# Kernel tuning notes

Measured on AMD Instinct MI355X. Metric: run time of the kernel, lower is better.

Reference implementation:

```python
import jax, jax.numpy as jnp
import numpy as np

E = 23   # unique experts
K = 3    # active experts per token

def setup_inputs() -> dict:
    key = jax.random.key(0)
    ks = jax.random.split(key, 11)
    d, h, B, N = 1024, 768, 16, 196
    s = 0.02  # init scale so sigmoid gate is non-saturated
    return {
        "x":      jax.random.normal(ks[0], (B, N, d), jnp.float32),
        "gate_w": jax.random.normal(ks[1], (d, E), jnp.float32) * s,
        "gate_b": jnp.zeros((E,), jnp.float32),
        "w1":     jax.random.normal(ks[2], (E, d, h), jnp.float32) * s,
        "b1":     jnp.zeros((E, h), jnp.float32),
        "w2":     jax.random.normal(ks[3], (E, h, d), jnp.float32) * s,
        "b2":     jnp.zeros((E, d), jnp.float32),
        "ws1":    jax.random.normal(ks[4], (d, h), jnp.float32) * s,
        "bs1":    jnp.zeros((h,), jnp.float32),
        "ws2":    jax.random.normal(ks[5], (h, d), jnp.float32) * s,
        "bs2":    jnp.zeros((d,), jnp.float32),
    }

def reference(x, gate_w, gate_b, w1, b1, w2, b2, ws1, bs1, ws2, bs2):
    o_shape = x.shape
    xt = x.reshape(-1, o_shape[-1])            # [T, d]
    T = xt.shape[0]

    # gating: sigmoid gate, top-3 (the 'bias' buffer in the source is zeros)
    gw = jax.nn.sigmoid(xt @ gate_w + gate_b)  # [T, E]
    top_vals, top_idx = jax.lax.top_k(gw, K)   # [T, K]
    tw = top_vals / top_vals.sum(-1, keepdims=True)

    # dense combine weights: tw scattered to [T, E] (0 for unselected experts)
    w_dense = jnp.zeros_like(gw).at[jnp.arange(T)[:, None], top_idx].add(tw)

    # expert MLPs (dense-masked equivalent of the grouped dispatch)
    hh = jax.nn.gelu(jnp.einsum('td,edh->teh', xt, w1) + b1, approximate=False)
    eo = jnp.einsum('teh,ehd->ted', hh, w2) + b2          # [T, E, d]

    # shared expert
    shared = jax.nn.gelu(xt @ ws1 + bs1, approximate=False) @ ws2 + bs2

    out = shared + jnp.einsum('ted,te->td', eo, w_dense)  # [T, d]

    # aux load-balancing loss
    gwn = gw / gw.sum(-1, keepdims=True)
    P = gwn.mean(0)                                       # [E]
    counts = jnp.zeros((E,), gw.dtype).at[top_idx.reshape(-1)].add(1.0)
    Fv = E * counts / (K * T)
    aux = (P * Fv).sum()

    return out.reshape(o_shape), aux
```

## Files before the change

### kernel.cpp

```cpp
#include <hip/hip_runtime.h>
#include <hip/hip_bf16.h>

#define T_TOK 3136
#define DDIM  1024
#define HDIM  768
#define NEXP  23
#define TOPK  3
#define MTILE 128
#define NTILE 128
#define KTILE 32
#define LDSB  40
#define MAXTILES 128
#define MAX_SLOTS 16384
#define GATE_BLOCKS 1568

typedef __attribute__((ext_vector_type(8))) short  short8;
typedef __attribute__((ext_vector_type(4))) short  short4v;
typedef __attribute__((ext_vector_type(4))) float  floatx4;

__device__ __forceinline__ short f2b(float f) {
    union { float f; unsigned u; } v; v.f = f;
    unsigned r = v.u + 0x7FFFu + ((v.u >> 16) & 1u);
    return (short)(r >> 16);
}
__device__ __forceinline__ float b2f(short s) {
    union { unsigned u; float f; } v; v.u = ((unsigned)(unsigned short)s) << 16; return v.f;
}
__device__ __forceinline__ float gelu_exact(float v) {
    return 0.5f * v * (1.0f + erff(v * 0.70710678118654752f));
}
__device__ __forceinline__ void gld16(const short* g, short* l) {
    __builtin_amdgcn_global_load_lds(
        (const __attribute__((address_space(1))) void*)g,
        (__attribute__((address_space(3))) void*)l, 16, 0, 0);
}

__global__ __launch_bounds__(256) void gwt_kernel(const float* __restrict__ gw, float* __restrict__ gwT) {
    __shared__ float tile[32][33];
    const int kt = blockIdx.x;
    const int tx = threadIdx.x & 31, ty = threadIdx.x >> 5;
    #pragma unroll
    for (int i = 0; i < 4; i++) {
        int k = ty + i * 8;
        tile[k][tx] = (tx < NEXP) ? gw[(size_t)(kt * 32 + k) * NEXP + tx] : 0.f;
    }
    __syncthreads();
    #pragma unroll
    for (int i = 0; i < 4; i++) {
        int e = ty + i * 8;
        if (e < 24) gwT[(size_t)e * DDIM + kt * 32 + tx] = tile[tx][e];
    }
}

__global__ __launch_bounds__(256) void xcvt_kernel(const float* __restrict__ x, short* __restrict__ xb) {
    int i = blockIdx.x * 256 + threadIdx.x;
    float4 v = ((const float4*)x)[i];
    short4v s = { f2b(v.x), f2b(v.y), f2b(v.z), f2b(v.w) };
    ((short4v*)xb)[i] = s;
}

__global__ __launch_bounds__(256) void gate_kernel(
    const float* __restrict__ x, const float* __restrict__ gwT, const float* __restrict__ gb,
    float* __restrict__ Pf, int* __restrict__ top_idx, float* __restrict__ top_w)
{
    const int tid = threadIdx.x;
    const int lane = tid & 63, wave = tid >> 6;
    const int ebase = wave * 6;
    __shared__ float sg[24];
    __shared__ float accP[NEXP];
    if (tid < NEXP) accP[tid] = 0.f;

    for (int t = blockIdx.x; t < T_TOK; t += GATE_BLOCKS) {
        const float4* xr4 = (const float4*)(x + (size_t)t * DDIM);
        float4 xv[4];
        #pragma unroll
        for (int j = 0; j < 4; j++) xv[j] = xr4[j * 64 + lane];

        double a0 = 0, a1 = 0, a2 = 0, a3 = 0, a4 = 0, a5 = 0;
        #pragma unroll
        for (int j = 0; j < 4; j++) {
            const float4* gp = (const float4*)gwT + (size_t)ebase * 256 + j * 64 + lane;
            float4 g0 = gp[0 * 256], g1 = gp[1 * 256], g2 = gp[2 * 256];
            float4 g3 = gp[3 * 256], g4 = gp[4 * 256], g5 = gp[5 * 256];
            float4 xj = xv[j];
            a0 += (double)xj.x * g0.x + (double)xj.y * g0.y + (double)xj.z * g0.z + (double)xj.w * g0.w;
            a1 += (double)xj.x * g1.x + (double)xj.y * g1.y + (double)xj.z * g1.z + (double)xj.w * g1.w;
            a2 += (double)xj.x * g2.x + (double)xj.y * g2.y + (double)xj.z * g2.z + (double)xj.w * g2.w;
            a3 += (double)xj.x * g3.x + (double)xj.y * g3.y + (double)xj.z * g3.z + (double)xj.w * g3.w;
            a4 += (double)xj.x * g4.x + (double)xj.y * g4.y + (double)xj.z * g4.z + (double)xj.w * g4.w;
            a5 += (double)xj.x * g5.x + (double)xj.y * g5.y + (double)xj.z * g5.z + (double)xj.w * g5.w;
        }
        #pragma unroll
        for (int off = 32; off > 0; off >>= 1) {
            a0 += __shfl_xor(a0, off);
            a1 += __shfl_xor(a1, off);
            a2 += __shfl_xor(a2, off);
            a3 += __shfl_xor(a3, off);
            a4 += __shfl_xor(a4, off);
            a5 += __shfl_xor(a5, off);
        }

        if (lane == 0) {
            double av[6] = { a0, a1, a2, a3, a4, a5 };
            #pragma unroll
            for (int i = 0; i < 6; i++) {
                int e = ebase + i;
                if (e < NEXP) {
                    float z = (float)av[i] + gb[e];
                    sg[e] = 1.0f / (1.0f + expf(-z));
                }
            }
        }
        __syncthreads();

        if (tid < NEXP) {
            float s = 0.f;
            #pragma unroll
            for (int e = 0; e < NEXP; e++) s += sg[e];
            accP[tid] += sg[tid] / s;
        }
        if (tid == 0) {
            float v0 = -1.f, v1 = -1.f, v2 = -1.f; int i0 = 0, i1 = 0, i2 = 0;
            for (int e = 0; e < NEXP; e++) {
                float v = sg[e];
                if (v > v0)      { v2 = v1; i2 = i1; v1 = v0; i1 = i0; v0 = v; i0 = e; }
                else if (v > v1) { v2 = v1; i2 = i1; v1 = v; i1 = e; }
                else if (v > v2) { v2 = v; i2 = e; }
            }
            float ts = v0 + v1 + v2;
            top_idx[t * 3 + 0] = i0; top_w[t * 3 + 0] = v0 / ts;
            top_idx[t * 3 + 1] = i1; top_w[t * 3 + 1] = v1 / ts;
            top_idx[t * 3 + 2] = i2; top_w[t * 3 + 2] = v2 / ts;
        }
        __syncthreads();
    }
    if (tid < NEXP) atomicAdd(&Pf[tid], accP[tid]);
}

__global__ __launch_bounds__(1024) void route_kernel(
    const int* __restrict__ top_idx, const float* __restrict__ Pf,
    int* __restrict__ ntl,
    int* __restrict__ slot_t, int* __restrict__ slot_of,
    int* __restrict__ tmap_e, int* __restrict__ tmap_b,
    float* __restrict__ out_aux)
{
    __shared__ int h[NEXP];
    __shared__ int lfill[NEXP];
    __shared__ int soffs[NEXP + 1];
    __shared__ int sntl[NEXP + 1];
    const int tid = threadIdx.x;
    if (tid < NEXP) { h[tid] = 0; lfill[tid] = 0; }
    __syncthreads();
    for (int i = tid; i < T_TOK * 3; i += 1024) atomicAdd(&h[top_idx[i]], 1);
    __syncthreads();
    if (tid == 0) {
        int o = 0, ti = 0;
        for (int e = 0; e < NEXP; e++) {
            int c = h[e];
            int nt = (c + MTILE - 1) / MTILE;
            soffs[e] = o; sntl[e] = nt; ntl[e] = nt;
            for (int j = 0; j < nt; j++) { tmap_e[ti] = e; tmap_b[ti] = o + j * MTILE; ti++; }
            o += nt * MTILE;
        }
        int nts = (T_TOK + MTILE - 1) / MTILE;
        soffs[NEXP] = o; sntl[NEXP] = nts; ntl[NEXP] = nts;
        for (int j = 0; j < nts; j++) { tmap_e[ti] = NEXP; tmap_b[ti] = o + j * MTILE; ti++; }
        ntl[NEXP + 1] = ti;
        float aux = 0.f;
        for (int e = 0; e < NEXP; e++) {
            float P = Pf[e] / (float)T_TOK;
            float F = (float)NEXP * (float)h[e] / (float)(TOPK * T_TOK);
            aux += P * F;
        }
        out_aux[0] = aux;
    }
    __syncthreads();
    for (int e = 0; e <= NEXP; e++) {
        int cnt = (e < NEXP) ? h[e] : T_TOK;
        int s0 = soffs[e] + cnt, s1 = soffs[e] + sntl[e] * MTILE;
        for (int s = s0 + tid; s < s1; s += 1024) slot_t[s] = 0;
    }
    for (int t = tid; t < T_TOK; t += 1024) {
        #pragma unroll
        for (int k = 0; k < TOPK; k++) {
            int e = top_idx[t * 3 + k];
            int pos = atomicAdd(&lfill[e], 1);
            int s = soffs[e] + pos;
            slot_t[s] = t;
            slot_of[t * 4 + k] = s;
        }
        int s = soffs[NEXP] + t;
        slot_t[s] = t;
        slot_of[t * 4 + 3] = s;
    }
}

__global__ __launch_bounds__(256) void gemm1_kernel(
    const short* __restrict__ xb,
    const float* __restrict__ w1, const float* __restrict__ b1,
    const float* __restrict__ ws1, const float* __restrict__ bs1,
    const int* __restrict__ tmap_e, const int* __restrict__ tmap_b,
    const int* __restrict__ ntl,
    const int* __restrict__ slot_t, short* __restrict__ hh)
{
    if ((int)blockIdx.y >= ntl[NEXP + 1]) return;
    const int e = tmap_e[blockIdx.y];
    const int slot_base = tmap_b[blockIdx.y];
    const int n0 = blockIdx.x * NTILE;
    const float* __restrict__ Wf = (e < NEXP) ? (w1 + (size_t)e * DDIM * HDIM) : ws1;
    const float* __restrict__ Bv = (e < NEXP) ? (b1 + (size_t)e * HDIM) : bs1;

    __shared__ __align__(16) short As[2][MTILE * KTILE];
    __shared__ __align__(16) short Bs[2][NTILE * LDSB];
    __shared__ int toks[MTILE];

    const int tid = threadIdx.x;
    for (int i = tid; i < MTILE; i += 256) toks[i] = slot_t[slot_base + i];

    const int lane = tid & 63, wave = tid >> 6;
    const int mbase = (wave & 1) * 64, nbase = (wave >> 1) * 64;
    const int lc = lane & 15, q = lane >> 4;
    const int xq8 = (q ^ ((lc >> 1) & 3)) << 3;

    const int srow = wave * 16 + (lane >> 2);
    const int c8   = (lane & 3) * 8;

    __syncthreads();
    const short* gA0 = xb + (size_t)toks[srow]      * DDIM + c8;
    const short* gA1 = xb + (size_t)toks[64 + srow] * DDIM + c8;
    const int lofs0 = wave * 512, lofs1 = 2048 + wave * 512;

    const int g = wave, cn = lane;
    const float* gW = Wf + (size_t)(8 * g) * HDIM + n0 + 2 * cn;
    const int bws = (g ^ (cn & 3)) << 3;
    const int bofs0 = (2 * cn) * LDSB + bws, bofs1 = (2 * cn + 1) * LDSB + bws;

    floatx4 acc[4][4];
    #pragma unroll
    for (int m = 0; m < 4; m++)
        #pragma unroll
        for (int n = 0; n < 4; n++) acc[m][n] = (floatx4)0.f;

    const int NT = DDIM / KTILE;
    float2 f[8];
    #pragma unroll
    for (int j = 0; j < 8; j++) f[j] = *(const float2*)(gW + (size_t)j * HDIM);
    gld16(gA0, &As[0][lofs0]);
    gld16(gA1, &As[0][lofs1]);
    {
        short8 s0, s1;
        #pragma unroll
        for (int j = 0; j < 8; j++) { s0[j] = f2b(f[j].x); s1[j] = f2b(f[j].y); }
        *(short8*)&Bs[0][bofs0] = s0;
        *(short8*)&Bs[0][bofs1] = s1;
    }
    #pragma unroll
    for (int j = 0; j < 8; j++) f[j] = *(const float2*)(gW + (size_t)(KTILE + j) * HDIM);
    __syncthreads();

    for (int t = 0; t < NT; t++) {
        const int cur = t & 1;
        if (t + 1 < NT) {
            gld16(gA0 + (t + 1) * KTILE, &As[cur ^ 1][lofs0]);
            gld16(gA1 + (t + 1) * KTILE, &As[cur ^ 1][lofs1]);
            short8 s0, s1;
            #pragma unroll
            for (int j = 0; j < 8; j++) { s0[j] = f2b(f[j].x); s1[j] = f2b(f[j].y); }
            *(short8*)&Bs[cur ^ 1][bofs0] = s0;
            *(short8*)&Bs[cur ^ 1][bofs1] = s1;
        }
        if (t + 2 < NT) {
            #pragma unroll
            for (int j = 0; j < 8; j++)
                f[j] = *(const float2*)(gW + (size_t)((t + 2) * KTILE + j) * HDIM);
        }
        short8 af[4], bf[4];
        #pragma unroll
        for (int m = 0; m < 4; m++) af[m] = *(const short8*)&As[cur][(mbase + m * 16 + lc) * KTILE + q * 8];
        #pragma unroll
        for (int n = 0; n < 4; n++) bf[n] = *(const short8*)&Bs[cur][(nbase + n * 16 + lc) * LDSB + xq8];
        #pragma unroll
        for (int m = 0; m < 4; m++)
            #pragma unroll
            for (int n = 0; n < 4; n++)
                acc[m][n] = __builtin_amdgcn_mfma_f32_16x16x32_bf16(af[m], bf[n], acc[m][n], 0, 0, 0);
        __syncthreads();
    }

    #pragma unroll
    for (int n = 0; n < 4; n++) {
        const int col = n0 + nbase + n * 16 + lc;
        const float bb = Bv[col];
        #pragma unroll
        for (int m = 0; m < 4; m++) {
            const int rbase = slot_base + mbase + m * 16 + q * 4;
            #pragma unroll
            for (int r = 0; r < 4; r++) {
                float v = acc[m][n][r] + bb;
                hh[(size_t)(rbase + r) * HDIM + col] = f2b(gelu_exact(v));
            }
        }
    }
}

__global__ __launch_bounds__(256) void gemm2_kernel(
    const short* __restrict__ hh,
    const float* __restrict__ w2, const float* __restrict__ b2,
    const float* __restrict__ ws2, const float* __restrict__ bs2,
    const int* __restrict__ tmap_e, const int* __restrict__ tmap_b,
    const int* __restrict__ ntl,
    short* __restrict__ eo)
{
    if ((int)blockIdx.y >= ntl[NEXP + 1]) return;
    const int e = tmap_e[blockIdx.y];
    const int slot_base = tmap_b[blockIdx.y];
    const int n0 = blockIdx.x * NTILE;
    const float* __restrict__ Wf = (e < NEXP) ? (w2 + (size_t)e * HDIM * DDIM) : ws2;
    const float* __restrict__ Bv = (e < NEXP) ? (b2 + (size_t)e * DDIM) : bs2;

    __shared__ __align__(16) short As[2][MTILE * KTILE];
    __shared__ __align__(16) short Bs[2][NTILE * LDSB];

    const int tid = threadIdx.x;
    const int lane = tid & 63, wave = tid >> 6;
    const int mbase = (wave & 1) * 64, nbase = (wave >> 1) * 64;
    const int lc = lane & 15, q = lane >> 4;
    const int xq8 = (q ^ ((lc >> 1) & 3)) << 3;

    const int srow = wave * 16 + (lane >> 2);
    const int c8   = (lane & 3) * 8;

    const short* gA0 = hh + (size_t)(slot_base + srow)      * HDIM + c8;
    const short* gA1 = hh + (size_t)(slot_base + 64 + srow) * HDIM + c8;
    const int lofs0 = wave * 512, lofs1 = 2048 + wave * 512;

    const int g = wave, cn = lane;
    const float* gW = Wf + (size_t)(8 * g) * DDIM + n0 + 2 * cn;
    const int bws = (g ^ (cn & 3)) << 3;
    const int bofs0 = (2 * cn) * LDSB + bws, bofs1 = (2 * cn + 1) * LDSB + bws;

    floatx4 acc[4][4];
    #pragma unroll
    for (int m = 0; m < 4; m++)
        #pragma unroll
        for (int n = 0; n < 4; n++) acc[m][n] = (floatx4)0.f;

    const int NT = HDIM / KTILE;
    float2 f[8];
    #pragma unroll
    for (int j = 0; j < 8; j++) f[j] = *(const float2*)(gW + (size_t)j * DDIM);
    gld16(gA0, &As[0][lofs0]);
    gld16(gA1, &As[0][lofs1]);
    {
        short8 s0, s1;
        #pragma unroll
        for (int j = 0; j < 8; j++) { s0[j] = f2b(f[j].x); s1[j] = f2b(f[j].y); }
        *(short8*)&Bs[0][bofs0] = s0;
        *(short8*)&Bs[0][bofs1] = s1;
    }
    #pragma unroll
    for (int j = 0; j < 8; j++) f[j] = *(const float2*)(gW + (size_t)(KTILE + j) * DDIM);
    __syncthreads();

    for (int t = 0; t < NT; t++) {
        const int cur = t & 1;
        if (t + 1 < NT) {
            gld16(gA0 + (t + 1) * KTILE, &As[cur ^ 1][lofs0]);
            gld16(gA1 + (t + 1) * KTILE, &As[cur ^ 1][lofs1]);
            short8 s0, s1;
            #pragma unroll
            for (int j = 0; j < 8; j++) { s0[j] = f2b(f[j].x); s1[j] = f2b(f[j].y); }
            *(short8*)&Bs[cur ^ 1][bofs0] = s0;
            *(short8*)&Bs[cur ^ 1][bofs1] = s1;
        }
        if (t + 2 < NT) {
            #pragma unroll
            for (int j = 0; j < 8; j++)
                f[j] = *(const float2*)(gW + (size_t)((t + 2) * KTILE + j) * DDIM);
        }
        short8 af[4], bf[4];
        #pragma unroll
        for (int m = 0; m < 4; m++) af[m] = *(const short8*)&As[cur][(mbase + m * 16 + lc) * KTILE + q * 8];
        #pragma unroll
        for (int n = 0; n < 4; n++) bf[n] = *(const short8*)&Bs[cur][(nbase + n * 16 + lc) * LDSB + xq8];
        #pragma unroll
        for (int m = 0; m < 4; m++)
            #pragma unroll
            for (int n = 0; n < 4; n++)
                acc[m][n] = __builtin_amdgcn_mfma_f32_16x16x32_bf16(af[m], bf[n], acc[m][n], 0, 0, 0);
        __syncthreads();
    }

    #pragma unroll
    for (int n = 0; n < 4; n++) {
        const int col = n0 + nbase + n * 16 + lc;
        const float bb = Bv[col];
        #pragma unroll
        for (int m = 0; m < 4; m++) {
            const int rbase = slot_base + mbase + m * 16 + q * 4;
            #pragma unroll
            for (int r = 0; r < 4; r++)
                eo[(size_t)(rbase + r) * DDIM + col] = f2b(acc[m][n][r] + bb);
        }
    }
}

__global__ __launch_bounds__(256) void combine_kernel(
    const short* __restrict__ eo, const float* __restrict__ top_w,
    const int* __restrict__ slot_of, float* __restrict__ out)
{
    const int t = blockIdx.x;
    const int c = threadIdx.x * 4;
    const int s0 = slot_of[t * 4 + 0], s1 = slot_of[t * 4 + 1];
    const int s2 = slot_of[t * 4 + 2], s3 = slot_of[t * 4 + 3];
    const float w0 = top_w[t * 3 + 0], w1 = top_w[t * 3 + 1], w2 = top_w[t * 3 + 2];
    short4v a = *(const short4v*)(eo + (size_t)s0 * DDIM + c);
    short4v b = *(const short4v*)(eo + (size_t)s1 * DDIM + c);
    short4v d = *(const short4v*)(eo + (size_t)s2 * DDIM + c);
    short4v s = *(const short4v*)(eo + (size_t)s3 * DDIM + c);
    float4 o;
    o.x = b2f(s.x) + w0 * b2f(a.x) + w1 * b2f(b.x) + w2 * b2f(d.x);
    o.y = b2f(s.y) + w0 * b2f(a.y) + w1 * b2f(b.y) + w2 * b2f(d.y);
    o.z = b2f(s.z) + w0 * b2f(a.z) + w1 * b2f(b.z) + w2 * b2f(d.z);
    o.w = b2f(s.w) + w0 * b2f(a.w) + w1 * b2f(b.w) + w2 * b2f(d.w);
    *(float4*)(out + (size_t)t * DDIM + c) = o;
}

extern "C" void kernel_launch(void* const* d_in, const int* in_sizes, int n_in,
                              void* d_out, int out_size, void* d_ws, size_t ws_size,
                              hipStream_t stream)
{
    const float* x   = (const float*)d_in[0];
    const float* gw  = (const float*)d_in[1];
    const float* gb  = (const float*)d_in[2];
    const float* w1  = (const float*)d_in[3];
    const float* b1  = (const float*)d_in[4];
    const float* w2  = (const float*)d_in[5];
    const float* b2  = (const float*)d_in[6];
    const float* ws1 = (const float*)d_in[7];
    const float* bs1 = (const float*)d_in[8];
    const float* ws2 = (const float*)d_in[9];
    const float* bs2 = (const float*)d_in[10];
    float* out = (float*)d_out;

    char* p = (char*)d_ws;
    auto alloc = [&](size_t bytes) -> char* {
        char* r = p; p += (bytes + 255) & ~(size_t)255; return r;
    };
    int*   top_idx  = (int*)  alloc((size_t)T_TOK * 3 * 4);
    float* top_w    = (float*)alloc((size_t)T_TOK * 3 * 4);
    float* Pf       = (float*)alloc(NEXP * 4);
    int*   ntl      = (int*)  alloc((NEXP + 2) * 4);
    int*   slot_t   = (int*)  alloc((size_t)MAX_SLOTS * 4);
    int*   slot_of  = (int*)  alloc((size_t)T_TOK * 4 * 4);
    int*   tmap_e   = (int*)  alloc((size_t)MAXTILES * 4);
    int*   tmap_b   = (int*)  alloc((size_t)MAXTILES * 4);
    float* gwT      = (float*)alloc((size_t)24 * DDIM * 4);
    short* xb       = (short*)alloc((size_t)T_TOK * DDIM * 2);
    short* hh       = (short*)alloc((size_t)MAX_SLOTS * HDIM * 2);
    short* eo       = (short*)alloc((size_t)MAX_SLOTS * DDIM * 2);

    hipMemsetAsync(Pf, 0, NEXP * 4, stream);

    gwt_kernel<<<DDIM / 32, 256, 0, stream>>>(gw, gwT);
    xcvt_kernel<<<(T_TOK * DDIM / 4) / 256, 256, 0, stream>>>(x, xb);
    gate_kernel<<<GATE_BLOCKS, 256, 0, stream>>>(x, gwT, gb, Pf, top_idx, top_w);
    route_kernel<<<1, 1024, 0, stream>>>(top_idx, Pf, ntl, slot_t, slot_of,
                                         tmap_e, tmap_b, out + (size_t)T_TOK * DDIM);
    gemm1_kernel<<<dim3(HDIM / NTILE, MAXTILES), 256, 0, stream>>>(
        xb, w1, b1, ws1, bs1, tmap_e, tmap_b, ntl, slot_t, hh);
    gemm2_kernel<<<dim3(DDIM / NTILE, MAXTILES), 256, 0, stream>>>(
        hh, w2, b2, ws2, bs2, tmap_e, tmap_b, ntl, eo);
    combine_kernel<<<T_TOK, 256, 0, stream>>>(eo, top_w, slot_of, out);
}
```

Measured before the change: 383.3 us.

## Double K-step per GEMM iteration and fuse prep kernels into one launch

Both expert GEMM kernels now process 64 K-elements per main-loop iteration as two 32-wide sub-tiles, halving the number of barriers and loop iterations and deepening the register prefetch of fp32 weights. The x-to-bf16 conversion and gate-weight transpose kernels are merged into a single launch to save one kernel launch. The change doubles LDS use per block and register pressure from the larger prefetch buffer, which may reduce occupancy.

```diff
diff --git a/kernel.cpp b/kernel.cpp
--- a/kernel.cpp
+++ b/kernel.cpp
@@ -9,10 +9,14 @@
 #define MTILE 128
 #define NTILE 128
 #define KTILE 32
+#define KSTEP 64
 #define LDSB  40
+#define ASUB  4096
+#define BSUB  5120
 #define MAXTILES 128
 #define MAX_SLOTS 16384
 #define GATE_BLOCKS 1568
+#define XCVT_BLOCKS 3136
 
 typedef __attribute__((ext_vector_type(8))) short  short8;
 typedef __attribute__((ext_vector_type(4))) short  short4v;
@@ -35,9 +39,19 @@
         (__attribute__((address_space(3))) void*)l, 16, 0, 0);
 }
 
-__global__ __launch_bounds__(256) void gwt_kernel(const float* __restrict__ gw, float* __restrict__ gwT) {
+__global__ __launch_bounds__(256) void prep_kernel(
+    const float* __restrict__ x, short* __restrict__ xb,
+    const float* __restrict__ gw, float* __restrict__ gwT)
+{
     __shared__ float tile[32][33];
-    const int kt = blockIdx.x;
+    if (blockIdx.x < XCVT_BLOCKS) {
+        int i = blockIdx.x * 256 + threadIdx.x;
+        float4 v = ((const float4*)x)[i];
+        short4v s = { f2b(v.x), f2b(v.y), f2b(v.z), f2b(v.w) };
+        ((short4v*)xb)[i] = s;
+        return;
+    }
+    const int kt = blockIdx.x - XCVT_BLOCKS;
     const int tx = threadIdx.x & 31, ty = threadIdx.x >> 5;
     #pragma unroll
     for (int i = 0; i < 4; i++) {
@@ -50,13 +64,6 @@
         int e = ty + i * 8;
         if (e < 24) gwT[(size_t)e * DDIM + kt * 32 + tx] = tile[tx][e];
     }
-}
-
-__global__ __launch_bounds__(256) void xcvt_kernel(const float* __restrict__ x, short* __restrict__ xb) {
-    int i = blockIdx.x * 256 + threadIdx.x;
-    float4 v = ((const float4*)x)[i];
-    short4v s = { f2b(v.x), f2b(v.y), f2b(v.z), f2b(v.w) };
-    ((short4v*)xb)[i] = s;
 }
 
 __global__ __launch_bounds__(256) void gate_kernel(
@@ -210,8 +217,8 @@
     const float* __restrict__ Wf = (e < NEXP) ? (w1 + (size_t)e * DDIM * HDIM) : ws1;
     const float* __restrict__ Bv = (e < NEXP) ? (b1 + (size_t)e * HDIM) : bs1;
 
-    __shared__ __align__(16) short As[2][MTILE * KTILE];
-    __shared__ __align__(16) short Bs[2][NTILE * LDSB];
+    __shared__ __align__(16) short As[2][2 * ASUB];
+    __shared__ __align__(16) short Bs[2][2 * BSUB];
     __shared__ int toks[MTILE];
 
     const int tid = threadIdx.x;
@@ -241,49 +248,78 @@
         #pragma unroll
         for (int n = 0; n < 4; n++) acc[m][n] = (floatx4)0.f;
 
-    const int NT = DDIM / KTILE;
-    float2 f[8];
-    #pragma unroll
-    for (int j = 0; j < 8; j++) f[j] = *(const float2*)(gW + (size_t)j * HDIM);
-    gld16(gA0, &As[0][lofs0]);
-    gld16(gA1, &As[0][lofs1]);
+    const int NT = DDIM / KSTEP;
+    float2 f[16];
+    #pragma unroll
+    for (int j = 0; j < 8; j++) {
+        f[j]     = *(const float2*)(gW + (size_t)j * HDIM);
+        f[8 + j] = *(const float2*)(gW + (size_t)(32 + j) * HDIM);
+    }
+    gld16(gA0,      &As[0][lofs0]);
+    gld16(gA1,      &As[0][lofs1]);
+    gld16(gA0 + 32, &As[0][ASUB + lofs0]);
+    gld16(gA1 + 32, &As[0][ASUB + lofs1]);
     {
-        short8 s0, s1;
-        #pragma unroll
-        for (int j = 0; j < 8; j++) { s0[j] = f2b(f[j].x); s1[j] = f2b(f[j].y); }
+        short8 s0, s1, s2, s3;
+        #pragma unroll
+        for (int j = 0; j < 8; j++) {
+            s0[j] = f2b(f[j].x);     s1[j] = f2b(f[j].y);
+            s2[j] = f2b(f[8 + j].x); s3[j] = f2b(f[8 + j].y);
+        }
         *(short8*)&Bs[0][bofs0] = s0;
         *(short8*)&Bs[0][bofs1] = s1;
-    }
-    #pragma unroll
-    for (int j = 0; j < 8; j++) f[j] = *(const float2*)(gW + (size_t)(KTILE + j) * HDIM);
+        *(short8*)&Bs[0][BSUB + bofs0] = s2;
+        *(short8*)&Bs[0][BSUB + bofs1] = s3;
+    }
+    #pragma unroll
+    for (int j = 0; j < 8; j++) {
+        f[j]     = *(const float2*)(gW + (size_t)(KSTEP + j) * HDIM);
+        f[8 + j] = *(const float2*)(gW + (size_t)(KSTEP + 32 + j) * HDIM);
+    }
     __syncthreads();
 
     for (int t = 0; t < NT; t++) {
         const int cur = t & 1;
         if (t + 1 < NT) {
-            gld16(gA0 + (t + 1) * KTILE, &As[cur ^ 1][lofs0]);
-            gld16(gA1 + (t + 1) * KTILE, &As[cur ^ 1][lofs1]);
-            short8 s0, s1;
-            #pragma unroll
-            for (int j = 0; j < 8; j++) { s0[j] = f2b(f[j].x); s1[j] = f2b(f[j].y); }
+            const int k1 = (t + 1) * KSTEP;
+            gld16(gA0 + k1,      &As[cur ^ 1][lofs0]);
+            gld16(gA1 + k1,      &As[cur ^ 1][lofs1]);
+            gld16(gA0 + k1 + 32, &As[cur ^ 1][ASUB + lofs0]);
+            gld16(gA1 + k1 + 32, &As[cur ^ 1][ASUB + lofs1]);
+            short8 s0, s1, s2, s3;
+            #pragma unroll
+            for (int j = 0; j < 8; j++) {
+                s0[j] = f2b(f[j].x);     s1[j] = f2b(f[j].y);
+                s2[j] = f2b(f[8 + j].x); s3[j] = f2b(f[8 + j].y);
+            }
             *(short8*)&Bs[cur ^ 1][bofs0] = s0;
             *(short8*)&Bs[cur ^ 1][bofs1] = s1;
+            *(short8*)&Bs[cur ^ 1][BSUB + bofs0] = s2;
+            *(short8*)&Bs[cur ^ 1][BSUB + bofs1] = s3;
         }
         if (t + 2 < NT) {
-            #pragma unroll
-            for (int j = 0; j < 8; j++)
-                f[j] = *(const float2*)(gW + (size_t)((t + 2) * KTILE + j) * HDIM);
-        }
-        short8 af[4], bf[4];
-        #pragma unroll
-        for (int m = 0; m < 4; m++) af[m] = *(const short8*)&As[cur][(mbase + m * 16 + lc) * KTILE + q * 8];
-        #pragma unroll
-        for (int n = 0; n < 4; n++) bf[n] = *(const short8*)&Bs[cur][(nbase + n * 16 + lc) * LDSB + xq8];
-        #pragma unroll
-        for (int m = 0; m < 4; m++)
+            const int k2 = (t + 2) * KSTEP;
+            #pragma unroll
+            for (int j = 0; j < 8; j++) {
+                f[j]     = *(const float2*)(gW + (size_t)(k2 + j) * HDIM);
+                f[8 + j] = *(const float2*)(gW + (size_t)(k2 + 32 + j) * HDIM);
+            }
+        }
+        #pragma unroll
+        for (int s = 0; s < 2; s++) {
+            short8 af[4], bf[4];
+            #pragma unroll
+            for (int m = 0; m < 4; m++)
+                af[m] = *(const short8*)&As[cur][s * ASUB + (mbase + m * 16 + lc) * KTILE + q * 8];
             #pragma unroll
             for (int n = 0; n < 4; n++)
-                acc[m][n] = __builtin_amdgcn_mfma_f32_16x16x32_bf16(af[m], bf[n], acc[m][n], 0, 0, 0);
+                bf[n] = *(const short8*)&Bs[cur][s * BSUB + (nbase + n * 16 + lc) * LDSB + xq8];
+            #pragma unroll
+            for (int m = 0; m < 4; m++)
+                #pragma unroll
+                for (int n = 0; n < 4; n++)
+                    acc[m][n] = __builtin_amdgcn_mfma_f32_16x16x32_bf16(af[m], bf[n], acc[m][n], 0, 0, 0);
+        }
         __syncthreads();
     }
 
@@ -318,8 +354,8 @@
     const float* __restrict__ Wf = (e < NEXP) ? (w2 + (size_t)e * HDIM * DDIM) : ws2;
     const float* __restrict__ Bv = (e < NEXP) ? (b2 + (size_t)e * DDIM) : bs2;
 
-    __shared__ __align__(16) short As[2][MTILE * KTILE];
-    __shared__ __align__(16) short Bs[2][NTILE * LDSB];
+    __shared__ __align__(16) short As[2][2 * ASUB];
+    __shared__ __align__(16) short Bs[2][2 * BSUB];
 
     const int tid = threadIdx.x;
     const int lane = tid & 63, wave = tid >> 6;
@@ -345,49 +381,78 @@
         #pragma unroll
         for (int n = 0; n < 4; n++) acc[m][n] = (floatx4)0.f;
 
-    const int NT = HDIM / KTILE;
-    float2 f[8];
-    #pragma unroll
-    for (int j = 0; j < 8; j++) f[j] = *(const float2*)(gW + (size_t)j * DDIM);
-    gld16(gA0, &As[0][lofs0]);
-    gld16(gA1, &As[0][lofs1]);
+    const int NT = HDIM / KSTEP;
+    float2 f[16];
+    #pragma unroll
+    for (int j = 0; j < 8; j++) {
+        f[j]     = *(const float2*)(gW + (size_t)j * DDIM);
+        f[8 + j] = *(const float2*)(gW + (size_t)(32 + j) * DDIM);
+    }
+    gld16(gA0,      &As[0][lofs0]);
+    gld16(gA1,      &As[0][lofs1]);
+    gld16(gA0 + 32, &As[0][ASUB + lofs0]);
+    gld16(gA1 + 32, &As[0][ASUB + lofs1]);
     {
-        short8 s0, s1;
-        #pragma unroll
-        for (int j = 0; j < 8; j++) { s0[j] = f2b(f[j].x); s1[j] = f2b(f[j].y); }
+        short8 s0, s1, s2, s3;
+        #pragma unroll
+        for (int j = 0; j < 8; j++) {
+            s0[j] = f2b(f[j].x);     s1[j] = f2b(f[j].y);
+            s2[j] = f2b(f[8 + j].x); s3[j] = f2b(f[8 + j].y);
+        }
         *(short8*)&Bs[0][bofs0] = s0;
         *(short8*)&Bs[0][bofs1] = s1;
-    }
-    #pragma unroll
-    for (int j = 0; j < 8; j++) f[j] = *(const float2*)(gW + (size_t)(KTILE + j) * DDIM);
+        *(short8*)&Bs[0][BSUB + bofs0] = s2;
+        *(short8*)&Bs[0][BSUB + bofs1] = s3;
+    }
+    #pragma unroll
+    for (int j = 0; j < 8; j++) {
+        f[j]     = *(const float2*)(gW + (size_t)(KSTEP + j) * DDIM);
+        f[8 + j] = *(const float2*)(gW + (size_t)(KSTEP + 32 + j) * DDIM);
+    }
     __syncthreads();
 
     for (int t = 0; t < NT; t++) {
         const int cur = t & 1;
         if (t + 1 < NT) {
-            gld16(gA0 + (t + 1) * KTILE, &As[cur ^ 1][lofs0]);
-            gld16(gA1 + (t + 1) * KTILE, &As[cur ^ 1][lofs1]);
-            short8 s0, s1;
-            #pragma unroll
-            for (int j = 0; j < 8; j++) { s0[j] = f2b(f[j].x); s1[j] = f2b(f[j].y); }
+            const int k1 = (t + 1) * KSTEP;
+            gld16(gA0 + k1,      &As[cur ^ 1][lofs0]);
+            gld16(gA1 + k1,      &As[cur ^ 1][lofs1]);
+            gld16(gA0 + k1 + 32, &As[cur ^ 1][ASUB + lofs0]);
+            gld16(gA1 + k1 + 32, &As[cur ^ 1][ASUB + lofs1]);
+            short8 s0, s1, s2, s3;
+            #pragma unroll
+            for (int j = 0; j < 8; j++) {
+                s0[j] = f2b(f[j].x);     s1[j] = f2b(f[j].y);
+                s2[j] = f2b(f[8 + j].x); s3[j] = f2b(f[8 + j].y);
+            }
             *(short8*)&Bs[cur ^ 1][bofs0] = s0;
             *(short8*)&Bs[cur ^ 1][bofs1] = s1;
+            *(short8*)&Bs[cur ^ 1][BSUB + bofs0] = s2;
+            *(short8*)&Bs[cur ^ 1][BSUB + bofs1] = s3;
         }
         if (t + 2 < NT) {
-            #pragma unroll
-            for (int j = 0; j < 8; j++)
-                f[j] = *(const float2*)(gW + (size_t)((t + 2) * KTILE + j) * DDIM);
-        }
-        short8 af[4], bf[4];
-        #pragma unroll
-        for (int m = 0; m < 4; m++) af[m] = *(const short8*)&As[cur][(mbase + m * 16 + lc) * KTILE + q * 8];
-        #pragma unroll
-        for (int n = 0; n < 4; n++) bf[n] = *(const short8*)&Bs[cur][(nbase + n * 16 + lc) * LDSB + xq8];
-        #pragma unroll
-        for (int m = 0; m < 4; m++)
+            const int k2 = (t + 2) * KSTEP;
+            #pragma unroll
+            for (int j = 0; j < 8; j++) {
+                f[j]     = *(const float2*)(gW + (size_t)(k2 + j) * DDIM);
+                f[8 + j] = *(const float2*)(gW + (size_t)(k2 + 32 + j) * DDIM);
+            }
+        }
+        #pragma unroll
+        for (int s = 0; s < 2; s++) {
+            short8 af[4], bf[4];
+            #pragma unroll
+            for (int m = 0; m < 4; m++)
+                af[m] = *(const short8*)&As[cur][s * ASUB + (mbase + m * 16 + lc) * KTILE + q * 8];
             #pragma unroll
             for (int n = 0; n < 4; n++)
-                acc[m][n] = __builtin_amdgcn_mfma_f32_16x16x32_bf16(af[m], bf[n], acc[m][n], 0, 0, 0);
+                bf[n] = *(const short8*)&Bs[cur][s * BSUB + (nbase + n * 16 + lc) * LDSB + xq8];
+            #pragma unroll
+            for (int m = 0; m < 4; m++)
+                #pragma unroll
+                for (int n = 0; n < 4; n++)
+                    acc[m][n] = __builtin_amdgcn_mfma_f32_16x16x32_bf16(af[m], bf[n], acc[m][n], 0, 0, 0);
+        }
         __syncthreads();
     }
 
@@ -462,8 +527,7 @@
 
     hipMemsetAsync(Pf, 0, NEXP * 4, stream);
 
-    gwt_kernel<<<DDIM / 32, 256, 0, stream>>>(gw, gwT);
-    xcvt_kernel<<<(T_TOK * DDIM / 4) / 256, 256, 0, stream>>>(x, xb);
+    prep_kernel<<<XCVT_BLOCKS + DDIM / 32, 256, 0, stream>>>(x, xb, gw, gwT);
     gate_kernel<<<GATE_BLOCKS, 256, 0, stream>>>(x, gwT, gb, Pf, top_idx, top_w);
     route_kernel<<<1, 1024, 0, stream>>>(top_idx, Pf, ntl, slot_t, slot_of,
                                          tmap_e, tmap_b, out + (size_t)T_TOK * DDIM);
```

Result: no change. 381.4 us (-0.5%).
